# Optimization experiments

Hardware: AMD Instinct MI355X
Metric: run time of the kernel (lower is better)

Reference implementation:

```python
import jax, jax.numpy as jnp
import numpy as np

EPS = 0.001  # additive floor applied after relu, as in the torch code


def setup_inputs() -> dict:
    key = jax.random.key(0)
    kA, kB, kW = jax.random.split(key, 3)
    M, N, C, H, W = 512, 64, 128, 8, 8
    A = jax.random.normal(kA, (M, C, H, W), dtype=jnp.float32)
    B = jax.random.normal(kB, (N, C, H, W), dtype=jnp.float32)
    Wg = jax.random.normal(kW, (C, C), dtype=jnp.float32) * 0.01  # Wg.data.normal_(0.0, 0.01)
    return {"A": A, "B": B, "Wg": Wg}


def reference(A, B, Wg):
    # Faithful vectorization of MIMOcom.get_source_dst_max(A, B, dir=True).
    # Torch loops i,j over HxW: B0 = B[:, i, j, :]; G = B0 @ Wg;
    # combination[m, n, p] = sum_c A[m, p, c] * G[n, c]; running max over (i, j).
    M, C, H, W = A.shape
    N = B.shape[0]
    P = H * W
    Af = jnp.transpose(A, (0, 2, 3, 1)).reshape(M, P, C)  # [M, P, C]
    Bf = jnp.transpose(B, (0, 2, 3, 1)).reshape(N, P, C)  # [N, Q, C]
    G = Bf @ Wg                                           # [N, Q, D]
    scores = jnp.einsum('mpd,nqd->mnpq', Af, G)           # [M, N, P, Q]
    comb_max = scores.max(axis=-1)                        # max over B positions q
    return jax.nn.relu(comb_max) + EPS                    # [M, N, P]
```

## Files before the change

kernel.cpp:

```cpp
#include <hip/hip_runtime.h>
#include <hip/hip_bf16.h>
#include <stdint.h>

typedef __attribute__((ext_vector_type(8))) short bf16x8;
typedef __attribute__((ext_vector_type(16))) float f32x16;
using bf16 = __hip_bfloat16;

static constexpr int Mdim = 512;
static constexpr int Ndim = 64;
static constexpr int Cdim = 128;
static constexpr int Pdim = 64;
static constexpr float EPS_ADD = 0.001f;

__device__ __forceinline__ void gll16(const void* gsrc, void* ldst) {
    const __attribute__((address_space(1))) unsigned int* g =
        (const __attribute__((address_space(1))) unsigned int*)gsrc;
    __attribute__((address_space(3))) unsigned int* l =
        (__attribute__((address_space(3))) unsigned int*)(uintptr_t)ldst;
    __builtin_amdgcn_global_load_lds(g, l, 16, 0, 0);
}

__global__ void prep_kernel(const float* __restrict__ A, const float* __restrict__ B,
                            const float* __restrict__ Wg,
                            bf16* __restrict__ Afrag, bf16* __restrict__ Gfrag) {
    __shared__ float lds[128 * 65];
    const int t = threadIdx.x;

    if (blockIdx.x < 512) {
        const int m = blockIdx.x;
        const float* __restrict__ Am = A + (size_t)m * (Cdim * Pdim);
#pragma unroll
        for (int i = 0; i < 8; ++i) {
            int v = t + i * 256;
            int gidx = v * 4;
            int c = gidx >> 6, p = gidx & 63;
            float4 val = *reinterpret_cast<const float4*>(Am + gidx);
            float* dst = &lds[c * 65 + p];
            dst[0] = val.x; dst[1] = val.y; dst[2] = val.z; dst[3] = val.w;
        }
        __syncthreads();

        unsigned* __restrict__ dst32 = (unsigned*)(Afrag + (size_t)m * 8192);
#pragma unroll
        for (int i = 0; i < 16; ++i) {
            int pr = t + i * 256;
            int p = pr >> 6;
            int c = (pr & 63) << 1;
            float f0 = lds[c * 65 + p];
            float f1 = lds[(c + 1) * 65 + p];
            union { bf16 hh[2]; unsigned u; } pk;
            pk.hh[0] = __float2bfloat16(f0);
            pk.hh[1] = __float2bfloat16(f1);
            int h = p >> 5, l31 = p & 31;
            int ks = c >> 4, hi = (c >> 3) & 1, e = c & 7;
            dst32[h * 2048 + ks * 256 + hi * 128 + l31 * 4 + (e >> 1)] = pk.u;
        }
    } else {
        const int nb = blockIdx.x - 512;
        const int n  = nb >> 2;
        const int q0 = (nb & 3) * 16;
        const float* __restrict__ Bn = B + (size_t)n * (Cdim * Pdim);
#pragma unroll
        for (int i = 0; i < 8; ++i) {
            int v = t + i * 256;
            int gidx = v * 4;
            int c = gidx >> 6, q = gidx & 63;
            float4 val = *reinterpret_cast<const float4*>(Bn + gidx);
            float* dst = &lds[c * 65 + q];
            dst[0] = val.x; dst[1] = val.y; dst[2] = val.z; dst[3] = val.w;
        }
        __syncthreads();

        const int d  = t & 127;
        const int qb = q0 + (t >> 7) * 8;
        float acc[8] = {0.f, 0.f, 0.f, 0.f, 0.f, 0.f, 0.f, 0.f};
        for (int c = 0; c < 128; ++c) {
            float w = Wg[c * 128 + d];
#pragma unroll
            for (int qi = 0; qi < 8; ++qi)
                acc[qi] = fmaf(lds[c * 65 + qb + qi], w, acc[qi]);
        }
        bf16* __restrict__ gdst = Gfrag + (size_t)n * 8192;
        const int ks = d >> 4, hi = (d >> 3) & 1, e = d & 7;
#pragma unroll
        for (int qi = 0; qi < 8; ++qi) {
            int q = qb + qi;
            int qt = q >> 5, l31 = q & 31;
            gdst[qt * 4096 + ks * 512 + hi * 256 + l31 * 8 + e] = __float2bfloat16(acc[qi]);
        }
    }
}

__global__ __launch_bounds__(256, 2)
void gemm_max_kernel(const bf16* __restrict__ Afrag, const bf16* __restrict__ Gfrag,
                     float* __restrict__ out) {
    __shared__ bf16 sG[4][8192];
    const int tid  = threadIdx.x;
    const int lane = tid & 63;
    const int wv   = tid >> 6;
    const int mi = wv >> 1, h = wv & 1;
    const int l31 = lane & 31, hi = lane >> 5;
    const int mg = blockIdx.x & 127;
    const int bn = blockIdx.x >> 7;
    const int m0 = mg * 4 + mi * 2;

    bf16x8 a[2][8];
#pragma unroll
    for (int u = 0; u < 2; ++u) {
        const bf16* Ap = Afrag + (size_t)(m0 + u) * 8192 + h * 4096 + lane * 8;
#pragma unroll
        for (int ks = 0; ks < 8; ++ks)
            a[u][ks] = *reinterpret_cast<const bf16x8*>(Ap + ks * 512);
    }
    {
        const char* Gsrc = (const char*)(Gfrag + (size_t)(bn * 4) * 8192);
#pragma unroll
        for (int i = 0; i < 16; ++i) {
            int f = (i * 256 + tid) * 16;
            gll16(Gsrc + f, (char*)sG + f);
        }
    }
    asm volatile("s_waitcnt vmcnt(0)" ::: "memory");
    __builtin_amdgcn_s_barrier();
    __builtin_amdgcn_sched_barrier(0);

    const f32x16 z16 = {0.f,0.f,0.f,0.f,0.f,0.f,0.f,0.f,0.f,0.f,0.f,0.f,0.f,0.f,0.f,0.f};
    f32x16 acc0, acc1;
    bf16x8 gf0[8], gf1[8];

    auto ldgf = [&](bf16x8 (&g)[8], const char* base) {
#pragma unroll
        for (int ks = 0; ks < 8; ++ks)
            g[ks] = *reinterpret_cast<const bf16x8*>(base + ks * 1024);
    };
    auto mmcl = [&](const bf16x8 (&gf)[8]) {
        acc0 = __builtin_amdgcn_mfma_f32_32x32x16_bf16(gf[0], a[0][0], z16, 0, 0, 0);
        acc1 = __builtin_amdgcn_mfma_f32_32x32x16_bf16(gf[0], a[1][0], z16, 0, 0, 0);
#pragma unroll
        for (int ks = 1; ks < 8; ++ks) {
            acc0 = __builtin_amdgcn_mfma_f32_32x32x16_bf16(gf[ks], a[0][ks], acc0, 0, 0, 0);
            acc1 = __builtin_amdgcn_mfma_f32_32x32x16_bf16(gf[ks], a[1][ks], acc1, 0, 0, 0);
        }
    };
    auto red16 = [&](const f32x16& v) -> float {
        float x0 = fmaxf(v[0], v[1]),  x1 = fmaxf(v[2], v[3]);
        float x2 = fmaxf(v[4], v[5]),  x3 = fmaxf(v[6], v[7]);
        float x4 = fmaxf(v[8], v[9]),  x5 = fmaxf(v[10], v[11]);
        float x6 = fmaxf(v[12], v[13]), x7 = fmaxf(v[14], v[15]);
        x0 = fmaxf(x0, x1); x2 = fmaxf(x2, x3);
        x4 = fmaxf(x4, x5); x6 = fmaxf(x6, x7);
        return fmaxf(fmaxf(x0, x2), fmaxf(x4, x6));
    };

#pragma unroll
    for (int s = 0; s < 4; ++s) {
        const char* gb = (const char*)sG + s * 16384 + lane * 16;
        ldgf(gf0, gb);
        ldgf(gf1, gb + 8192);
        mmcl(gf0);
        float t0 = red16(acc0), t1 = red16(acc1);
        mmcl(gf1);
        t0 = fmaxf(t0, red16(acc0));
        t1 = fmaxf(t1, red16(acc1));
        t0 = fmaxf(t0, __shfl_xor(t0, 32));
        t1 = fmaxf(t1, __shfl_xor(t1, 32));
        const int n = bn * 4 + s;
        const float sv = hi ? t1 : t0;
        out[(size_t)(m0 + hi) * 4096 + n * 64 + h * 32 + l31] =
            fmaxf(sv, 0.f) + EPS_ADD;
    }
}

extern "C" void kernel_launch(void* const* d_in, const int* in_sizes, int n_in,
                              void* d_out, int out_size, void* d_ws, size_t ws_size,
                              hipStream_t stream) {
    const float* A  = (const float*)d_in[0];
    const float* B  = (const float*)d_in[1];
    const float* Wg = (const float*)d_in[2];
    float* out = (float*)d_out;

    bf16* Afrag = (bf16*)d_ws;
    bf16* Gfrag = (bf16*)((char*)d_ws + (size_t)Mdim * Pdim * Cdim * sizeof(bf16));

    prep_kernel<<<768, 256, 0, stream>>>(A, B, Wg, Afrag, Gfrag);
    gemm_max_kernel<<<2048, 256, 0, stream>>>(Afrag, Gfrag, out);
}
```

Before: 45.40 us.

## Reuse staged G tile across four M groups with double-buffered A loads

Each block now handles 16 rows of M (four groups of four) instead of four, so the G tile staged in LDS is reused four times and the grid shrinks from 2048 to 512 blocks. A fragments for the next group are prefetched into a second register buffer while the current group runs its MFMA work, hiding global load latency. In exchange there are fewer blocks (512 across the CUs, limiting parallelism) and more registers per thread from holding two A buffers, which could lower occupancy.

```diff
diff --git a/kernel.cpp b/kernel.cpp
--- a/kernel.cpp
+++ b/kernel.cpp
@@ -100,18 +100,24 @@
     const int wv   = tid >> 6;
     const int mi = wv >> 1, h = wv & 1;
     const int l31 = lane & 31, hi = lane >> 5;
-    const int mg = blockIdx.x & 127;
-    const int bn = blockIdx.x >> 7;
-    const int m0 = mg * 4 + mi * 2;
-
-    bf16x8 a[2][8];
-#pragma unroll
-    for (int u = 0; u < 2; ++u) {
-        const bf16* Ap = Afrag + (size_t)(m0 + u) * 8192 + h * 4096 + lane * 8;
-#pragma unroll
-        for (int ks = 0; ks < 8; ++ks)
-            a[u][ks] = *reinterpret_cast<const bf16x8*>(Ap + ks * 512);
-    }
+    const int mgo = blockIdx.x & 31;
+    const int bn  = blockIdx.x >> 5;
+
+    const bf16* Awave = Afrag + (size_t)h * 4096 + lane * 8;
+
+    auto loadA = [&](bf16x8 (&dst)[2][8], int g) {
+        const int mb = mgo * 16 + g * 4 + mi * 2;
+#pragma unroll
+        for (int u = 0; u < 2; ++u) {
+            const bf16* Ap = Awave + (size_t)(mb + u) * 8192;
+#pragma unroll
+            for (int ks = 0; ks < 8; ++ks)
+                dst[u][ks] = *reinterpret_cast<const bf16x8*>(Ap + ks * 512);
+        }
+    };
+
+    bf16x8 aA[2][8], aB[2][8];
+    loadA(aA, 0);
     {
         const char* Gsrc = (const char*)(Gfrag + (size_t)(bn * 4) * 8192);
 #pragma unroll
@@ -126,22 +132,7 @@
 
     const f32x16 z16 = {0.f,0.f,0.f,0.f,0.f,0.f,0.f,0.f,0.f,0.f,0.f,0.f,0.f,0.f,0.f,0.f};
     f32x16 acc0, acc1;
-    bf16x8 gf0[8], gf1[8];
-
-    auto ldgf = [&](bf16x8 (&g)[8], const char* base) {
-#pragma unroll
-        for (int ks = 0; ks < 8; ++ks)
-            g[ks] = *reinterpret_cast<const bf16x8*>(base + ks * 1024);
-    };
-    auto mmcl = [&](const bf16x8 (&gf)[8]) {
-        acc0 = __builtin_amdgcn_mfma_f32_32x32x16_bf16(gf[0], a[0][0], z16, 0, 0, 0);
-        acc1 = __builtin_amdgcn_mfma_f32_32x32x16_bf16(gf[0], a[1][0], z16, 0, 0, 0);
-#pragma unroll
-        for (int ks = 1; ks < 8; ++ks) {
-            acc0 = __builtin_amdgcn_mfma_f32_32x32x16_bf16(gf[ks], a[0][ks], acc0, 0, 0, 0);
-            acc1 = __builtin_amdgcn_mfma_f32_32x32x16_bf16(gf[ks], a[1][ks], acc1, 0, 0, 0);
-        }
-    };
+
     auto red16 = [&](const f32x16& v) -> float {
         float x0 = fmaxf(v[0], v[1]),  x1 = fmaxf(v[2], v[3]);
         float x2 = fmaxf(v[4], v[5]),  x3 = fmaxf(v[6], v[7]);
@@ -152,23 +143,51 @@
         return fmaxf(fmaxf(x0, x2), fmaxf(x4, x6));
     };
 
-#pragma unroll
-    for (int s = 0; s < 4; ++s) {
-        const char* gb = (const char*)sG + s * 16384 + lane * 16;
-        ldgf(gf0, gb);
-        ldgf(gf1, gb + 8192);
-        mmcl(gf0);
-        float t0 = red16(acc0), t1 = red16(acc1);
-        mmcl(gf1);
-        t0 = fmaxf(t0, red16(acc0));
-        t1 = fmaxf(t1, red16(acc1));
-        t0 = fmaxf(t0, __shfl_xor(t0, 32));
-        t1 = fmaxf(t1, __shfl_xor(t1, 32));
-        const int n = bn * 4 + s;
-        const float sv = hi ? t1 : t0;
-        out[(size_t)(m0 + hi) * 4096 + n * 64 + h * 32 + l31] =
-            fmaxf(sv, 0.f) + EPS_ADD;
-    }
+    auto group = [&](const bf16x8 (&a)[2][8], int g) {
+        const int mb = mgo * 16 + g * 4 + mi * 2;
+#pragma unroll
+        for (int s = 0; s < 4; ++s) {
+            const char* gb = (const char*)sG + s * 16384 + lane * 16;
+            bf16x8 gf0[8], gf1[8];
+#pragma unroll
+            for (int ks = 0; ks < 8; ++ks)
+                gf0[ks] = *reinterpret_cast<const bf16x8*>(gb + ks * 1024);
+#pragma unroll
+            for (int ks = 0; ks < 8; ++ks)
+                gf1[ks] = *reinterpret_cast<const bf16x8*>(gb + 8192 + ks * 1024);
+            acc0 = __builtin_amdgcn_mfma_f32_32x32x16_bf16(gf0[0], a[0][0], z16, 0, 0, 0);
+            acc1 = __builtin_amdgcn_mfma_f32_32x32x16_bf16(gf0[0], a[1][0], z16, 0, 0, 0);
+#pragma unroll
+            for (int ks = 1; ks < 8; ++ks) {
+                acc0 = __builtin_amdgcn_mfma_f32_32x32x16_bf16(gf0[ks], a[0][ks], acc0, 0, 0, 0);
+                acc1 = __builtin_amdgcn_mfma_f32_32x32x16_bf16(gf0[ks], a[1][ks], acc1, 0, 0, 0);
+            }
+            float t0 = red16(acc0), t1 = red16(acc1);
+            acc0 = __builtin_amdgcn_mfma_f32_32x32x16_bf16(gf1[0], a[0][0], z16, 0, 0, 0);
+            acc1 = __builtin_amdgcn_mfma_f32_32x32x16_bf16(gf1[0], a[1][0], z16, 0, 0, 0);
+#pragma unroll
+            for (int ks = 1; ks < 8; ++ks) {
+                acc0 = __builtin_amdgcn_mfma_f32_32x32x16_bf16(gf1[ks], a[0][ks], acc0, 0, 0, 0);
+                acc1 = __builtin_amdgcn_mfma_f32_32x32x16_bf16(gf1[ks], a[1][ks], acc1, 0, 0, 0);
+            }
+            t0 = fmaxf(t0, red16(acc0));
+            t1 = fmaxf(t1, red16(acc1));
+            t0 = fmaxf(t0, __shfl_xor(t0, 32));
+            t1 = fmaxf(t1, __shfl_xor(t1, 32));
+            const int n = bn * 4 + s;
+            const float sv = hi ? t1 : t0;
+            out[(size_t)(mb + hi) * 4096 + n * 64 + h * 32 + l31] =
+                fmaxf(sv, 0.f) + EPS_ADD;
+        }
+    };
+
+    loadA(aB, 1);
+    group(aA, 0);
+    loadA(aA, 2);
+    group(aB, 1);
+    loadA(aB, 3);
+    group(aA, 2);
+    group(aB, 3);
 }
 
 extern "C" void kernel_launch(void* const* d_in, const int* in_sizes, int n_in,
@@ -183,5 +202,5 @@
     bf16* Gfrag = (bf16*)((char*)d_ws + (size_t)Mdim * Pdim * Cdim * sizeof(bf16));
 
     prep_kernel<<<768, 256, 0, stream>>>(A, B, Wg, Afrag, Gfrag);
-    gemm_max_kernel<<<2048, 256, 0, stream>>>(Afrag, Gfrag, out);
-}
+    gemm_max_kernel<<<512, 256, 0, stream>>>(Afrag, Gfrag, out);
+}
```

New measurement: 49.00 us. 1.08x slower.
